# Kernel optimization log

Hardware: AMD Instinct MI355X
Metric: run time of the kernel (lower is better)

Reference implementation:

```python
import jax, jax.numpy as jnp
import numpy as np

D_MODEL = 1024
N_HEADS = 16
HEAD_DIM = D_MODEL // N_HEADS
SEQ_LEN = 2048
D_FF = 4 * D_MODEL
LCC_SCALE = 0.1
LN_EPS = 1e-5
NORM_EPS = 1e-12  # F.normalize eps


def _layer_norm(x, g, b):
    mu = jnp.mean(x, axis=-1, keepdims=True)
    var = jnp.mean(jnp.square(x - mu), axis=-1, keepdims=True)
    return (x - mu) * jax.lax.rsqrt(var + LN_EPS) * g + b


def setup_inputs() -> dict:
    key = jax.random.key(0)
    ks = jax.random.split(key, 8)
    s = 0.02  # weight init scale
    return {
        "x": jax.random.normal(ks[0], (SEQ_LEN, D_MODEL), jnp.float32),
        "lcc_values": jax.random.uniform(ks[1], (SEQ_LEN,), jnp.float32),
        "w_qkv": jax.random.normal(ks[2], (D_MODEL, 3 * D_MODEL), jnp.float32) * s,
        "b_qkv": jnp.zeros((3 * D_MODEL,), jnp.float32),
        "w_out": jax.random.normal(ks[3], (D_MODEL, D_MODEL), jnp.float32) * s,
        "b_out": jnp.zeros((D_MODEL,), jnp.float32),
        "ln1_g": jnp.ones((D_MODEL,), jnp.float32),
        "ln1_b": jnp.zeros((D_MODEL,), jnp.float32),
        "ln2_g": jnp.ones((D_MODEL,), jnp.float32),
        "ln2_b": jnp.zeros((D_MODEL,), jnp.float32),
        "w_ff1": jax.random.normal(ks[4], (D_MODEL, D_FF), jnp.float32) * s,
        "b_ff1": jnp.zeros((D_FF,), jnp.float32),
        "w_ff2": jax.random.normal(ks[5], (D_FF, D_MODEL), jnp.float32) * s,
        "b_ff2": jnp.zeros((D_MODEL,), jnp.float32),
    }


def reference(x, lcc_values, w_qkv, b_qkv, w_out, b_out, ln1_g, ln1_b,
              ln2_g, ln2_b, w_ff1, b_ff1, w_ff2, b_ff2):
    L = x.shape[0]
    scaling = HEAD_DIM ** -0.5

    normed = _layer_norm(x, ln1_g, ln1_b)
    qkv = normed @ w_qkv + b_qkv                      # [L, 3D]
    qkv = qkv.reshape(L, 3, N_HEADS, HEAD_DIM)
    q = jnp.transpose(qkv[:, 0], (1, 0, 2))           # [H, L, d]
    k = jnp.transpose(qkv[:, 1], (1, 0, 2))
    v = jnp.transpose(qkv[:, 2], (1, 0, 2))

    # cosine attention: L2-normalize q, k
    q = q / jnp.maximum(jnp.linalg.norm(q, axis=-1, keepdims=True), NORM_EPS)
    k = k / jnp.maximum(jnp.linalg.norm(k, axis=-1, keepdims=True), NORM_EPS)
    q = q * scaling

    scores = jnp.einsum('hld,hmd->hlm', q, k)         # [H, L, L]
    bias = (lcc_values[:, None] + lcc_values[None, :]) * 0.5 * LCC_SCALE
    scores = jnp.clip(scores + bias[None], -10.0, 10.0)
    probs = jax.nn.softmax(scores, axis=-1)

    attn = jnp.einsum('hlm,hmd->hld', probs, v)       # [H, L, d]
    attn = jnp.transpose(attn, (1, 0, 2)).reshape(L, D_MODEL)
    x = x + (attn @ w_out + b_out)

    normed2 = _layer_norm(x, ln2_g, ln2_b)
    h = jax.nn.gelu(normed2 @ w_ff1 + b_ff1, approximate=False)
    x = x + (h @ w_ff2 + b_ff2)
    return x
```

## Files before the change

### kernel.cpp

```cpp
#include <hip/hip_runtime.h>
#include <hip/hip_bf16.h>

#define D_MODEL 1024
#define SEQ 2048
#define NH 16
#define HD 64
#define DFF 4096

typedef __attribute__((ext_vector_type(8))) __bf16 bf16x8;
typedef __attribute__((ext_vector_type(4))) float f32x4;

__device__ __forceinline__ unsigned short f2bf(float f) {
    union { float f; unsigned u; } v; v.f = f;
    unsigned r = v.u + 0x7fffu + ((v.u >> 16) & 1u);
    return (unsigned short)(r >> 16);
}
__device__ __forceinline__ unsigned pack2(float a, float b) {
    return (unsigned)f2bf(a) | ((unsigned)f2bf(b) << 16);
}
__device__ __forceinline__ float bf2f(unsigned short u) {
    union { unsigned u; float f; } v; v.u = ((unsigned)u) << 16;
    return v.f;
}
__device__ __forceinline__ bf16x8 ld_frag(const unsigned short* p) {
    union { uint4 u; bf16x8 b; } c;
    c.u = *(const uint4*)p;
    return c.b;
}
__device__ __forceinline__ void load16(const float* p, float* v) {
#pragma unroll
    for (int i = 0; i < 4; i++) {
        float4 f = ((const float4*)p)[i];
        v[4*i+0]=f.x; v[4*i+1]=f.y; v[4*i+2]=f.z; v[4*i+3]=f.w;
    }
}

typedef __attribute__((address_space(3))) unsigned lds_u32;
typedef const __attribute__((address_space(1))) unsigned glob_u32;
__device__ __forceinline__ void gl_lds16(const unsigned short* g, unsigned short* l) {
    __builtin_amdgcn_global_load_lds((glob_u32*)g, (lds_u32*)l, 16, 0, 0);
}

#define MFMA16(a,b,c) __builtin_amdgcn_mfma_f32_16x16x32_bf16(a,b,c,0,0,0)

__global__ __launch_bounds__(256) void wcast_t(const float* __restrict__ W,
                                               unsigned short* __restrict__ Wt,
                                               int K, int N) {
    __shared__ unsigned short lt[64][72];
    int t = threadIdx.x;
    int nb = blockIdx.x, kb = blockIdx.y;
    int r = t >> 2, c0 = (t & 3) << 4;
    const float* src = W + (size_t)(kb*64 + r) * N + nb*64 + c0;
    float4 f0 = ((const float4*)src)[0];
    float4 f1 = ((const float4*)src)[1];
    float4 f2 = ((const float4*)src)[2];
    float4 f3 = ((const float4*)src)[3];
    unsigned* dst = (unsigned*)&lt[r][c0];
    dst[0]=pack2(f0.x,f0.y); dst[1]=pack2(f0.z,f0.w);
    dst[2]=pack2(f1.x,f1.y); dst[3]=pack2(f1.z,f1.w);
    dst[4]=pack2(f2.x,f2.y); dst[5]=pack2(f2.z,f2.w);
    dst[6]=pack2(f3.x,f3.y); dst[7]=pack2(f3.z,f3.w);
    __syncthreads();
    int n_ = t >> 2, k0 = (t & 3) << 4;
    unsigned obuf[8];
#pragma unroll
    for (int i = 0; i < 8; i++)
        obuf[i] = (unsigned)lt[k0 + 2*i][n_] | ((unsigned)lt[k0 + 2*i + 1][n_] << 16);
    unsigned short* out = Wt + (size_t)(nb*64 + n_) * K + kb*64 + k0;
    ((uint4*)out)[0] = *(uint4*)&obuf[0];
    ((uint4*)out)[1] = *(uint4*)&obuf[4];
}

__global__ __launch_bounds__(256) void ln_kernel(const float* __restrict__ x,
                                                 const float* __restrict__ g,
                                                 const float* __restrict__ b,
                                                 unsigned short* __restrict__ out) {
    int row = blockIdx.x, t = threadIdx.x;
    float4 v = ((const float4*)(x + (size_t)row * D_MODEL))[t];
    float s  = v.x + v.y + v.z + v.w;
    float sq = v.x*v.x + v.y*v.y + v.z*v.z + v.w*v.w;
#pragma unroll
    for (int m = 1; m < 64; m <<= 1) { s += __shfl_xor(s, m, 64); sq += __shfl_xor(sq, m, 64); }
    __shared__ float ls[4], lq[4];
    int wave = t >> 6, lane = t & 63;
    if (lane == 0) { ls[wave] = s; lq[wave] = sq; }
    __syncthreads();
    s  = ls[0]+ls[1]+ls[2]+ls[3];
    sq = lq[0]+lq[1]+lq[2]+lq[3];
    float mu  = s * (1.0f / D_MODEL);
    float var = sq * (1.0f / D_MODEL) - mu * mu;
    float rs  = rsqrtf(var + 1e-5f);
    int c = t * 4;
    float y0 = (v.x - mu) * rs * g[c+0] + b[c+0];
    float y1 = (v.y - mu) * rs * g[c+1] + b[c+1];
    float y2 = (v.z - mu) * rs * g[c+2] + b[c+2];
    float y3 = (v.w - mu) * rs * g[c+3] + b[c+3];
    unsigned* o = (unsigned*)(out + (size_t)row * D_MODEL + c);
    o[0] = pack2(y0, y1); o[1] = pack2(y2, y3);
}

template<int NP>
__device__ __forceinline__ void reduce_body(const float* __restrict__ res,
                                            const float* __restrict__ bias,
                                            const unsigned short* __restrict__ parts,
                                            float* __restrict__ out,
                                            int MN, int Ndiv4) {
    int i = blockIdx.x * 256 + threadIdx.x;
    float4 r = ((const float4*)res)[i];
    float4 b = ((const float4*)bias)[i & (Ndiv4 - 1)];
    r.x += b.x; r.y += b.y; r.z += b.z; r.w += b.w;
#pragma unroll
    for (int p = 0; p < NP; p++) {
        ushort4 u = ((const ushort4*)(parts + (size_t)p * MN))[i];
        r.x += bf2f(u.x); r.y += bf2f(u.y); r.z += bf2f(u.z); r.w += bf2f(u.w);
    }
    ((float4*)out)[i] = r;
}
__global__ __launch_bounds__(256) void reduce_op(const float* res, const float* bias,
                                                 const unsigned short* parts, float* out,
                                                 int MN, int Ndiv4) {
    reduce_body<2>(res, bias, parts, out, MN, Ndiv4);
}
__global__ __launch_bounds__(256) void reduce_ff2(const float* res, const float* bias,
                                                  const unsigned short* parts, float* out,
                                                  int MN, int Ndiv4) {
    reduce_body<4>(res, bias, parts, out, MN, Ndiv4);
}

template<int TM, int TN, int SPLITK, int GELU, int RES, int OUTBF, int PART>
__device__ __forceinline__ void gemm_body(const unsigned short* __restrict__ A,
                                          const unsigned short* __restrict__ Bt,
                                          const float* __restrict__ bias,
                                          const float* __restrict__ res,
                                          void* __restrict__ C,
                                          int M, int N, int K) {
    constexpr int AI = TM / 32;
    constexpr int BI = TN / 32;
    constexpr int MI = TM / 32;
    constexpr int NI = TN / 32;
    constexpr int HALF = (TM + TN) * 64;
    __shared__ unsigned short smem[2 * HALF];
    int t = threadIdx.x;
    int bn = blockIdx.x, bm = blockIdx.y;
    int kz = (SPLITK > 1) ? blockIdx.z : 0;
    int KS = K / SPLITK;
    int K0 = kz * KS;
    int wave = t >> 6, lane = t & 63;
    int quad = lane >> 4, lr = lane & 15;

    const unsigned short* pa[AI];
    int aoff[AI];
#pragma unroll
    for (int i = 0; i < AI; i++) {
        int rl = wave*(TM/4) + i*8 + (lane >> 3);
        int ss = (lane & 7) ^ (rl & 7);
        pa[i] = A + (size_t)(bm*TM + rl) * K + K0 + ss*8;
        aoff[i] = (wave*(TM/4) + i*8) * 64;
    }
    const unsigned short* pb[BI];
    int boff[BI];
#pragma unroll
    for (int i = 0; i < BI; i++) {
        int rl = wave*(TN/4) + i*8 + (lane >> 3);
        int ss = (lane & 7) ^ (rl & 7);
        pb[i] = Bt + (size_t)(bn*TN + rl) * K + K0 + ss*8;
        boff[i] = TM*64 + (wave*(TN/4) + i*8) * 64;
    }

    int wr = (wave >> 1) * (TM/2), wc = (wave & 1) * (TN/2);
    int foA[2][MI], foB[2][NI];
#pragma unroll
    for (int i = 0; i < MI; i++) {
        int row = wr + i*16 + lr;
        foA[0][i] = row*64 + ((quad     ^ (row & 7)))*8;
        foA[1][i] = row*64 + (((quad+4) ^ (row & 7)))*8;
    }
#pragma unroll
    for (int j = 0; j < NI; j++) {
        int row = wc + j*16 + lr;
        foB[0][j] = TM*64 + row*64 + ((quad     ^ (row & 7)))*8;
        foB[1][j] = TM*64 + row*64 + (((quad+4) ^ (row & 7)))*8;
    }

    f32x4 z = {0.f, 0.f, 0.f, 0.f};
    f32x4 acc[MI][NI];
#pragma unroll
    for (int i = 0; i < MI; i++)
#pragma unroll
        for (int j = 0; j < NI; j++) acc[i][j] = z;

#pragma unroll
    for (int i = 0; i < AI; i++) gl_lds16(pa[i], smem + aoff[i]);
#pragma unroll
    for (int i = 0; i < BI; i++) gl_lds16(pb[i], smem + boff[i]);

    int bo = 0;
    for (int kk = 0; kk < KS; kk += 64) {
        __syncthreads();
        if (kk + 64 < KS) {
            int nb = bo ^ HALF;
#pragma unroll
            for (int i = 0; i < AI; i++) gl_lds16(pa[i] + kk + 64, smem + nb + aoff[i]);
#pragma unroll
            for (int i = 0; i < BI; i++) gl_lds16(pb[i] + kk + 64, smem + nb + boff[i]);
        }
#pragma unroll
        for (int h = 0; h < 2; h++) {
            bf16x8 af[MI], bfr[NI];
#pragma unroll
            for (int i = 0; i < MI; i++) af[i]  = ld_frag(smem + bo + foA[h][i]);
#pragma unroll
            for (int j = 0; j < NI; j++) bfr[j] = ld_frag(smem + bo + foB[h][j]);
#pragma unroll
            for (int i = 0; i < MI; i++)
#pragma unroll
                for (int j = 0; j < NI; j++)
                    acc[i][j] = MFMA16(af[i], bfr[j], acc[i][j]);
        }
        bo ^= HALF;
    }

    if (PART) {
        unsigned short* P = (unsigned short*)C + (size_t)kz * M * N;
#pragma unroll
        for (int i = 0; i < MI; i++)
#pragma unroll
            for (int j = 0; j < NI; j++) {
                int row0 = bm*TM + wr + i*16 + quad*4;
                int col  = bn*TN + wc + j*16 + lr;
#pragma unroll
                for (int r = 0; r < 4; r++)
                    P[(size_t)(row0 + r) * N + col] = f2bf(acc[i][j][r]);
            }
    } else {
#pragma unroll
        for (int i = 0; i < MI; i++)
#pragma unroll
            for (int j = 0; j < NI; j++) {
                int row0 = bm*TM + wr + i*16 + quad*4;
                int col  = bn*TN + wc + j*16 + lr;
                float bv = bias[col];
#pragma unroll
                for (int r = 0; r < 4; r++) {
                    float v = acc[i][j][r] + bv;
                    if (RES)  v += res[(size_t)(row0 + r) * N + col];
                    if (GELU) v = 0.5f * v * (1.0f + erff(v * 0.70710678118654752f));
                    if (OUTBF) ((unsigned short*)C)[(size_t)(row0 + r) * N + col] = f2bf(v);
                    else       ((float*)C)[(size_t)(row0 + r) * N + col] = v;
                }
            }
    }
}

__global__ __launch_bounds__(256) void k_gemm_qkv(const unsigned short* A, const unsigned short* Bt,
                                                  const float* bias, float* C, int M, int N, int K) {
    gemm_body<128,64,1,0,0,0,0>(A, Bt, bias, nullptr, C, M, N, K);
}
__global__ __launch_bounds__(256) void k_gemm_op(const unsigned short* A, const unsigned short* Bt,
                                                 unsigned short* C, int M, int N, int K) {
    gemm_body<128,64,2,0,0,0,1>(A, Bt, nullptr, nullptr, C, M, N, K);
}
__global__ __launch_bounds__(256) void k_gemm_ff1(const unsigned short* A, const unsigned short* Bt,
                                                  const float* bias, unsigned short* C, int M, int N, int K) {
    gemm_body<128,64,1,1,0,1,0>(A, Bt, bias, nullptr, C, M, N, K);
}
__global__ __launch_bounds__(256) void k_gemm_ff2(const unsigned short* A, const unsigned short* Bt,
                                                  unsigned short* C, int M, int N, int K) {
    gemm_body<128,64,4,0,0,0,1>(A, Bt, nullptr, nullptr, C, M, N, K);
}

__global__ __launch_bounds__(256) void qkv_post(const float* __restrict__ qkv,
                                                unsigned short* __restrict__ qn,
                                                unsigned short* __restrict__ kn,
                                                unsigned short* __restrict__ vt) {
    __shared__ unsigned short lv[64][72];
    int h = blockIdx.x, lb = blockIdx.y;
    int t = threadIdx.x;
    int lloc = t >> 2, seg = (t & 3) << 4;
    int lg = lb*64 + lloc;
    const float* row = qkv + (size_t)lg * 3072;
    float vq[16], vk[16], vv[16];
    load16(row + h*64 + seg, vq);
    load16(row + 1024 + h*64 + seg, vk);
    load16(row + 2048 + h*64 + seg, vv);
    float sq = 0.f, sk = 0.f;
#pragma unroll
    for (int i = 0; i < 16; i++) { sq += vq[i]*vq[i]; sk += vk[i]*vk[i]; }
    sq += __shfl_xor(sq, 1, 64); sq += __shfl_xor(sq, 2, 64);
    sk += __shfl_xor(sk, 1, 64); sk += __shfl_xor(sk, 2, 64);
    float scq = 0.125f / fmaxf(sqrtf(sq), 1e-12f);
    float sck = 1.0f   / fmaxf(sqrtf(sk), 1e-12f);
    unsigned* oq = (unsigned*)(qn + ((size_t)h*SEQ + lg)*HD + seg);
    unsigned* ok = (unsigned*)(kn + ((size_t)h*SEQ + lg)*HD + seg);
#pragma unroll
    for (int i = 0; i < 8; i++) {
        oq[i] = pack2(vq[2*i]*scq, vq[2*i+1]*scq);
        ok[i] = pack2(vk[2*i]*sck, vk[2*i+1]*sck);
    }
    unsigned* lvp = (unsigned*)&lv[lloc][seg];
#pragma unroll
    for (int i = 0; i < 8; i++) lvp[i] = pack2(vv[2*i], vv[2*i+1]);
    __syncthreads();
    int dloc = t >> 2, l0 = (t & 3) << 4;
    unsigned obuf[8];
#pragma unroll
    for (int i = 0; i < 8; i++)
        obuf[i] = (unsigned)lv[l0 + 2*i][dloc] | ((unsigned)lv[l0 + 2*i + 1][dloc] << 16);
    unsigned short* ov = vt + ((size_t)h*HD + dloc)*SEQ + lb*64 + l0;
    ((uint4*)ov)[0] = *(uint4*)&obuf[0];
    ((uint4*)ov)[1] = *(uint4*)&obuf[4];
}

#define KSPLIT 2
#define KTILES (SEQ / 64 / KSPLIT)
__global__ __launch_bounds__(256) void attn_kernel(const unsigned short* __restrict__ qn,
                                                   const unsigned short* __restrict__ kn,
                                                   const unsigned short* __restrict__ vt,
                                                   const float* __restrict__ lcc,
                                                   float* __restrict__ num_ws,
                                                   float* __restrict__ den_ws) {
    __shared__ unsigned short lQ[64][72];
    __shared__ unsigned short lK[64][72];
    __shared__ unsigned short lV[64][72];
    __shared__ unsigned short lP[64][72];
    __shared__ float lL[SEQ / KSPLIT];
    int h = blockIdx.x, qb = blockIdx.y, kz = blockIdx.z;
    int t = threadIdx.x;
    int rl = t >> 2, c0 = (t & 3) << 4;
    const unsigned short* pq = qn + ((size_t)h*SEQ + qb*64 + rl)*HD + c0;
    *(uint4*)&lQ[rl][c0]     = ((const uint4*)pq)[0];
    *(uint4*)&lQ[rl][c0 + 8] = ((const uint4*)pq)[1];
    for (int i = t; i < SEQ/KSPLIT; i += 256) lL[i] = 0.05f * lcc[kz*(SEQ/KSPLIT) + i];
    __syncthreads();
    int wave = t >> 6, lane = t & 63, quad = lane >> 4, lr = lane & 15;
    float lqv[4];
#pragma unroll
    for (int r = 0; r < 4; r++) lqv[r] = 0.05f * lcc[qb*64 + wave*16 + quad*4 + r];
    bf16x8 aq0 = ld_frag(&lQ[wave*16 + lr][quad*8]);
    bf16x8 aq1 = ld_frag(&lQ[wave*16 + lr][32 + quad*8]);
    f32x4 z = {0.f, 0.f, 0.f, 0.f};
    f32x4 oacc[4]; oacc[0]=z; oacc[1]=z; oacc[2]=z; oacc[3]=z;
    float den[4] = {0.f, 0.f, 0.f, 0.f};

    const unsigned short* kn0 = kn + (size_t)h*SEQ*HD + (size_t)kz*(SEQ/KSPLIT)*HD;
    const unsigned short* vt0 = vt + (size_t)h*HD*SEQ + kz*(SEQ/KSPLIT);

    for (int kb = 0; kb < KTILES; kb++) {
        __syncthreads();
        const unsigned short* pk = kn0 + (size_t)(kb*64 + rl)*HD + c0;
        uint4 k0v = ((const uint4*)pk)[0], k1v = ((const uint4*)pk)[1];
        const unsigned short* pv = vt0 + (size_t)rl*SEQ + kb*64 + c0;
        uint4 v0v = ((const uint4*)pv)[0], v1v = ((const uint4*)pv)[1];
        *(uint4*)&lK[rl][c0]     = k0v; *(uint4*)&lK[rl][c0 + 8] = k1v;
        *(uint4*)&lV[rl][c0]     = v0v; *(uint4*)&lV[rl][c0 + 8] = v1v;
        __syncthreads();
#pragma unroll
        for (int j = 0; j < 4; j++) {
            bf16x8 b0 = ld_frag(&lK[j*16 + lr][quad*8]);
            bf16x8 b1 = ld_frag(&lK[j*16 + lr][32 + quad*8]);
            f32x4 s = z;
            s = MFMA16(aq0, b0, s);
            s = MFMA16(aq1, b1, s);
            float lm = lL[kb*64 + j*16 + lr];
#pragma unroll
            for (int r = 0; r < 4; r++) {
                float sv = s[r] + lqv[r] + lm;
                sv = fminf(fmaxf(sv, -10.f), 10.f);
                float p = __expf(sv);
                den[r] += p;
                lP[wave*16 + quad*4 + r][j*16 + lr] = f2bf(p);
            }
        }
        bf16x8 ap0 = ld_frag(&lP[wave*16 + lr][quad*8]);
        bf16x8 ap1 = ld_frag(&lP[wave*16 + lr][32 + quad*8]);
#pragma unroll
        for (int j2 = 0; j2 < 4; j2++) {
            bf16x8 b0 = ld_frag(&lV[j2*16 + lr][quad*8]);
            bf16x8 b1 = ld_frag(&lV[j2*16 + lr][32 + quad*8]);
            oacc[j2] = MFMA16(ap0, b0, oacc[j2]);
            oacc[j2] = MFMA16(ap1, b1, oacc[j2]);
        }
    }
#pragma unroll
    for (int r = 0; r < 4; r++)
#pragma unroll
        for (int m = 1; m < 16; m <<= 1) den[r] += __shfl_xor(den[r], m, 64);

    float* nump = num_ws + (((size_t)(h*32 + qb)) * KSPLIT + kz) * 4096;
#pragma unroll
    for (int j2 = 0; j2 < 4; j2++)
#pragma unroll
        for (int r = 0; r < 4; r++)
            nump[(wave*16 + quad*4 + r) * 64 + j2*16 + lr] = oacc[j2][r];
    if (lr == 0) {
        float* denp = den_ws + (((size_t)(h*32 + qb)) * KSPLIT + kz) * 64;
#pragma unroll
        for (int r = 0; r < 4; r++) denp[wave*16 + quad*4 + r] = den[r];
    }
}

__global__ __launch_bounds__(256) void attn_comb(const float* __restrict__ num_ws,
                                                 const float* __restrict__ den_ws,
                                                 unsigned short* __restrict__ attn) {
    int hq = blockIdx.x;
    int h = hq >> 5, qb = hq & 31;
    int t = threadIdx.x;
    int row = t >> 2, col0 = (t & 3) << 4;
    const float* n0 = num_ws + ((size_t)hq * KSPLIT) * 4096 + row*64 + col0;
    const float* n1 = n0 + 4096;
    float d = den_ws[(size_t)hq * KSPLIT * 64 + row] + den_ws[((size_t)hq * KSPLIT + 1) * 64 + row];
    float inv = 1.0f / d;
    unsigned ob[8];
#pragma unroll
    for (int i = 0; i < 4; i++) {
        float4 a = ((const float4*)n0)[i];
        float4 b = ((const float4*)n1)[i];
        ob[2*i]   = pack2((a.x + b.x) * inv, (a.y + b.y) * inv);
        ob[2*i+1] = pack2((a.z + b.z) * inv, (a.w + b.w) * inv);
    }
    unsigned short* op = attn + (size_t)(qb*64 + row) * D_MODEL + h*64 + col0;
    ((uint4*)op)[0] = *(uint4*)&ob[0];
    ((uint4*)op)[1] = *(uint4*)&ob[4];
}

extern "C" void kernel_launch(void* const* d_in, const int* in_sizes, int n_in,
                              void* d_out, int out_size, void* d_ws, size_t ws_size,
                              hipStream_t stream) {
    const float* x      = (const float*)d_in[0];
    const float* lcc    = (const float*)d_in[1];
    const float* w_qkv  = (const float*)d_in[2];
    const float* b_qkv  = (const float*)d_in[3];
    const float* w_out  = (const float*)d_in[4];
    const float* b_out  = (const float*)d_in[5];
    const float* ln1_g  = (const float*)d_in[6];
    const float* ln1_b  = (const float*)d_in[7];
    const float* ln2_g  = (const float*)d_in[8];
    const float* ln2_b  = (const float*)d_in[9];
    const float* w_ff1  = (const float*)d_in[10];
    const float* b_ff1  = (const float*)d_in[11];
    const float* w_ff2  = (const float*)d_in[12];
    const float* b_ff2  = (const float*)d_in[13];

    char* ws = (char*)d_ws;
    unsigned short* wtq  = (unsigned short*)(ws);
    unsigned short* wto  = (unsigned short*)(ws + 6291456);
    unsigned short* wtf1 = (unsigned short*)(ws + 8388608);
    unsigned short* wtf2 = (unsigned short*)(ws + 16777216);
    unsigned short* xn   = (unsigned short*)(ws + 25165824);
    float*          qkvb = (float*)(ws + 29360128);
    float*          x1   = (float*)(ws + 29360128);
    float*          numw = (float*)(ws + 29360128);
    float*          denw = (float*)(ws + 46137344);
    unsigned short* hbuf = (unsigned short*)(ws + 37748736);
    unsigned short* pOP  = (unsigned short*)(ws + 37748736);
    unsigned short* qnb  = (unsigned short*)(ws + 54525952);
    unsigned short* knb  = (unsigned short*)(ws + 58720256);
    unsigned short* vtb  = (unsigned short*)(ws + 62914560);
    unsigned short* pFF2 = (unsigned short*)(ws);
    unsigned short* attnb = xn;
    unsigned short* x2n  = qnb;
    float* outp = (float*)d_out;


    wcast_t<<<dim3(48, 16), 256, 0, stream>>>(w_qkv, wtq, 1024, 3072);
    wcast_t<<<dim3(16, 16), 256, 0, stream>>>(w_out, wto, 1024, 1024);
    wcast_t<<<dim3(64, 16), 256, 0, stream>>>(w_ff1, wtf1, 1024, 4096);
    wcast_t<<<dim3(16, 64), 256, 0, stream>>>(w_ff2, wtf2, 4096, 1024);
    ln_kernel<<<SEQ, 256, 0, stream>>>(x, ln1_g, ln1_b, xn);
    k_gemm_qkv<<<dim3(48, 16), 256, 0, stream>>>(xn, wtq, b_qkv, qkvb, SEQ, 3072, 1024);
    qkv_post<<<dim3(16, 32), 256, 0, stream>>>(qkvb, qnb, knb, vtb);
    attn_kernel<<<dim3(16, 32, KSPLIT), 256, 0, stream>>>(qnb, knb, vtb, lcc, numw, denw);
    attn_comb<<<512, 256, 0, stream>>>(numw, denw, attnb);
    k_gemm_op<<<dim3(16, 16, 2), 256, 0, stream>>>(attnb, wto, pOP, SEQ, 1024, 1024);
    reduce_op<<<SEQ*D_MODEL/1024, 256, 0, stream>>>(x, b_out, pOP, x1, SEQ*D_MODEL, D_MODEL/4);
    ln_kernel<<<SEQ, 256, 0, stream>>>(x1, ln2_g, ln2_b, x2n);
    k_gemm_ff1<<<dim3(64, 16), 256, 0, stream>>>(x2n, wtf1, b_ff1, hbuf, SEQ, 4096, 1024);
    k_gemm_ff2<<<dim3(16, 16, 4), 256, 0, stream>>>(hbuf, wtf2, pFF2, SEQ, 1024, 4096);
    reduce_ff2<<<SEQ*D_MODEL/1024, 256, 0, stream>>>(x1, b_ff2, pFF2, outp, SEQ*D_MODEL, D_MODEL/4);
}
```

Baseline: 283.1 us.

## Fuse QKV post-processing into GEMM epilogue, merge weight casts and reduce+LN

```diff
diff --git a/kernel.cpp b/kernel.cpp
--- a/kernel.cpp
+++ b/kernel.cpp
@@ -27,13 +27,6 @@
     c.u = *(const uint4*)p;
     return c.b;
 }
-__device__ __forceinline__ void load16(const float* p, float* v) {
-#pragma unroll
-    for (int i = 0; i < 4; i++) {
-        float4 f = ((const float4*)p)[i];
-        v[4*i+0]=f.x; v[4*i+1]=f.y; v[4*i+2]=f.z; v[4*i+3]=f.w;
-    }
-}
 
 typedef __attribute__((address_space(3))) unsigned lds_u32;
 typedef const __attribute__((address_space(1))) unsigned glob_u32;
@@ -43,12 +36,18 @@
 
 #define MFMA16(a,b,c) __builtin_amdgcn_mfma_f32_16x16x32_bf16(a,b,c,0,0,0)
 
-__global__ __launch_bounds__(256) void wcast_t(const float* __restrict__ W,
-                                               unsigned short* __restrict__ Wt,
-                                               int K, int N) {
+__global__ __launch_bounds__(256) void wcast_all(const float* __restrict__ wq, const float* __restrict__ wo,
+                                                 const float* __restrict__ wf1, const float* __restrict__ wf2,
+                                                 unsigned short* __restrict__ oq, unsigned short* __restrict__ oo,
+                                                 unsigned short* __restrict__ of1, unsigned short* __restrict__ of2) {
     __shared__ unsigned short lt[64][72];
+    int id = blockIdx.x;
+    const float* W; unsigned short* O; int K, N, nb, kb;
+    if (id < 768)       { W = wq;  O = oq;  K = 1024; N = 3072; nb = id % 48; kb = id / 48; }
+    else if (id < 1024) { id -= 768;  W = wo;  O = oo;  K = 1024; N = 1024; nb = id & 15; kb = id >> 4; }
+    else if (id < 2048) { id -= 1024; W = wf1; O = of1; K = 1024; N = 4096; nb = id & 63; kb = id >> 6; }
+    else                { id -= 2048; W = wf2; O = of2; K = 4096; N = 1024; nb = id & 15; kb = id >> 4; }
     int t = threadIdx.x;
-    int nb = blockIdx.x, kb = blockIdx.y;
     int r = t >> 2, c0 = (t & 3) << 4;
     const float* src = W + (size_t)(kb*64 + r) * N + nb*64 + c0;
     float4 f0 = ((const float4*)src)[0];
@@ -66,7 +65,7 @@
 #pragma unroll
     for (int i = 0; i < 8; i++)
         obuf[i] = (unsigned)lt[k0 + 2*i][n_] | ((unsigned)lt[k0 + 2*i + 1][n_] << 16);
-    unsigned short* out = Wt + (size_t)(nb*64 + n_) * K + kb*64 + k0;
+    unsigned short* out = O + (size_t)(nb*64 + n_) * K + kb*64 + k0;
     ((uint4*)out)[0] = *(uint4*)&obuf[0];
     ((uint4*)out)[1] = *(uint4*)&obuf[4];
 }
@@ -99,75 +98,95 @@
     o[0] = pack2(y0, y1); o[1] = pack2(y2, y3);
 }
 
-template<int NP>
-__device__ __forceinline__ void reduce_body(const float* __restrict__ res,
-                                            const float* __restrict__ bias,
-                                            const unsigned short* __restrict__ parts,
-                                            float* __restrict__ out,
-                                            int MN, int Ndiv4) {
+__global__ __launch_bounds__(256) void reduce_ln(const float* __restrict__ x,
+                                                 const float* __restrict__ bout,
+                                                 const unsigned short* __restrict__ parts,
+                                                 const float* __restrict__ g,
+                                                 const float* __restrict__ b,
+                                                 float* __restrict__ x1,
+                                                 unsigned short* __restrict__ x2n) {
+    int row = blockIdx.x, t = threadIdx.x;
+    int i = row * 256 + t;
+    float4 v = ((const float4*)x)[i];
+    float4 bb = ((const float4*)bout)[t];
+    v.x += bb.x; v.y += bb.y; v.z += bb.z; v.w += bb.w;
+    ushort4 u0 = ((const ushort4*)parts)[i];
+    ushort4 u1 = ((const ushort4*)(parts + (size_t)SEQ*D_MODEL))[i];
+    v.x += bf2f(u0.x) + bf2f(u1.x);
+    v.y += bf2f(u0.y) + bf2f(u1.y);
+    v.z += bf2f(u0.z) + bf2f(u1.z);
+    v.w += bf2f(u0.w) + bf2f(u1.w);
+    ((float4*)x1)[i] = v;
+    float s  = v.x + v.y + v.z + v.w;
+    float sq = v.x*v.x + v.y*v.y + v.z*v.z + v.w*v.w;
+#pragma unroll
+    for (int m = 1; m < 64; m <<= 1) { s += __shfl_xor(s, m, 64); sq += __shfl_xor(sq, m, 64); }
+    __shared__ float ls[4], lq[4];
+    int wave = t >> 6, lane = t & 63;
+    if (lane == 0) { ls[wave] = s; lq[wave] = sq; }
+    __syncthreads();
+    s  = ls[0]+ls[1]+ls[2]+ls[3];
+    sq = lq[0]+lq[1]+lq[2]+lq[3];
+    float mu  = s * (1.0f / D_MODEL);
+    float var = sq * (1.0f / D_MODEL) - mu * mu;
+    float rs  = rsqrtf(var + 1e-5f);
+    int c = t * 4;
+    float y0 = (v.x - mu) * rs * g[c+0] + b[c+0];
+    float y1 = (v.y - mu) * rs * g[c+1] + b[c+1];
+    float y2 = (v.z - mu) * rs * g[c+2] + b[c+2];
+    float y3 = (v.w - mu) * rs * g[c+3] + b[c+3];
+    unsigned* o = (unsigned*)(x2n + (size_t)row * D_MODEL + c);
+    o[0] = pack2(y0, y1); o[1] = pack2(y2, y3);
+}
+
+__global__ __launch_bounds__(256) void reduce_ff2(const float* __restrict__ res,
+                                                  const float* __restrict__ bias,
+                                                  const unsigned short* __restrict__ parts,
+                                                  float* __restrict__ out) {
     int i = blockIdx.x * 256 + threadIdx.x;
     float4 r = ((const float4*)res)[i];
-    float4 b = ((const float4*)bias)[i & (Ndiv4 - 1)];
+    float4 b = ((const float4*)bias)[i & (D_MODEL/4 - 1)];
     r.x += b.x; r.y += b.y; r.z += b.z; r.w += b.w;
 #pragma unroll
-    for (int p = 0; p < NP; p++) {
-        ushort4 u = ((const ushort4*)(parts + (size_t)p * MN))[i];
+    for (int p = 0; p < 4; p++) {
+        ushort4 u = ((const ushort4*)(parts + (size_t)p * SEQ * D_MODEL))[i];
         r.x += bf2f(u.x); r.y += bf2f(u.y); r.z += bf2f(u.z); r.w += bf2f(u.w);
     }
     ((float4*)out)[i] = r;
 }
-__global__ __launch_bounds__(256) void reduce_op(const float* res, const float* bias,
-                                                 const unsigned short* parts, float* out,
-                                                 int MN, int Ndiv4) {
-    reduce_body<2>(res, bias, parts, out, MN, Ndiv4);
-}
-__global__ __launch_bounds__(256) void reduce_ff2(const float* res, const float* bias,
-                                                  const unsigned short* parts, float* out,
-                                                  int MN, int Ndiv4) {
-    reduce_body<4>(res, bias, parts, out, MN, Ndiv4);
-}
-
-template<int TM, int TN, int SPLITK, int GELU, int RES, int OUTBF, int PART>
-__device__ __forceinline__ void gemm_body(const unsigned short* __restrict__ A,
+
+#define TMg 128
+#define TNg 64
+#define SMEM_U16 (2 * (TMg + TNg) * 64)
+__device__ __forceinline__ void gemm_core(const unsigned short* __restrict__ A,
                                           const unsigned short* __restrict__ Bt,
-                                          const float* __restrict__ bias,
-                                          const float* __restrict__ res,
-                                          void* __restrict__ C,
-                                          int M, int N, int K) {
-    constexpr int AI = TM / 32;
-    constexpr int BI = TN / 32;
-    constexpr int MI = TM / 32;
-    constexpr int NI = TN / 32;
-    constexpr int HALF = (TM + TN) * 64;
-    __shared__ unsigned short smem[2 * HALF];
-    int t = threadIdx.x;
-    int bn = blockIdx.x, bm = blockIdx.y;
-    int kz = (SPLITK > 1) ? blockIdx.z : 0;
-    int KS = K / SPLITK;
-    int K0 = kz * KS;
-    int wave = t >> 6, lane = t & 63;
+                                          int K, int K0, int KS, int bm, int bn,
+                                          unsigned short* smem, f32x4 acc[4][2],
+                                          int wave, int lane) {
+    constexpr int AI = 4, BI = 2, MI = 4, NI = 2;
+    constexpr int HALF = (TMg + TNg) * 64;
     int quad = lane >> 4, lr = lane & 15;
 
     const unsigned short* pa[AI];
     int aoff[AI];
 #pragma unroll
     for (int i = 0; i < AI; i++) {
-        int rl = wave*(TM/4) + i*8 + (lane >> 3);
+        int rl = wave*32 + i*8 + (lane >> 3);
         int ss = (lane & 7) ^ (rl & 7);
-        pa[i] = A + (size_t)(bm*TM + rl) * K + K0 + ss*8;
-        aoff[i] = (wave*(TM/4) + i*8) * 64;
+        pa[i] = A + (size_t)(bm*TMg + rl) * K + K0 + ss*8;
+        aoff[i] = (wave*32 + i*8) * 64;
     }
     const unsigned short* pb[BI];
     int boff[BI];
 #pragma unroll
     for (int i = 0; i < BI; i++) {
-        int rl = wave*(TN/4) + i*8 + (lane >> 3);
+        int rl = wave*16 + i*8 + (lane >> 3);
         int ss = (lane & 7) ^ (rl & 7);
-        pb[i] = Bt + (size_t)(bn*TN + rl) * K + K0 + ss*8;
-        boff[i] = TM*64 + (wave*(TN/4) + i*8) * 64;
-    }
-
-    int wr = (wave >> 1) * (TM/2), wc = (wave & 1) * (TN/2);
+        pb[i] = Bt + (size_t)(bn*TNg + rl) * K + K0 + ss*8;
+        boff[i] = TMg*64 + (wave*16 + i*8) * 64;
+    }
+
+    int wr = (wave >> 1) * 64, wc = (wave & 1) * 32;
     int foA[2][MI], foB[2][NI];
 #pragma unroll
     for (int i = 0; i < MI; i++) {
@@ -178,16 +197,9 @@
 #pragma unroll
     for (int j = 0; j < NI; j++) {
         int row = wc + j*16 + lr;
-        foB[0][j] = TM*64 + row*64 + ((quad     ^ (row & 7)))*8;
-        foB[1][j] = TM*64 + row*64 + (((quad+4) ^ (row & 7)))*8;
-    }
-
-    f32x4 z = {0.f, 0.f, 0.f, 0.f};
-    f32x4 acc[MI][NI];
-#pragma unroll
-    for (int i = 0; i < MI; i++)
-#pragma unroll
-        for (int j = 0; j < NI; j++) acc[i][j] = z;
+        foB[0][j] = TMg*64 + row*64 + ((quad     ^ (row & 7)))*8;
+        foB[1][j] = TMg*64 + row*64 + (((quad+4) ^ (row & 7)))*8;
+    }
 
 #pragma unroll
     for (int i = 0; i < AI; i++) gl_lds16(pa[i], smem + aoff[i]);
@@ -219,96 +231,146 @@
         }
         bo ^= HALF;
     }
-
-    if (PART) {
-        unsigned short* P = (unsigned short*)C + (size_t)kz * M * N;
-#pragma unroll
-        for (int i = 0; i < MI; i++)
-#pragma unroll
-            for (int j = 0; j < NI; j++) {
-                int row0 = bm*TM + wr + i*16 + quad*4;
-                int col  = bn*TN + wc + j*16 + lr;
-#pragma unroll
-                for (int r = 0; r < 4; r++)
-                    P[(size_t)(row0 + r) * N + col] = f2bf(acc[i][j][r]);
+}
+
+__device__ __forceinline__ void acc_init(f32x4 acc[4][2]) {
+    f32x4 z = {0.f, 0.f, 0.f, 0.f};
+#pragma unroll
+    for (int i = 0; i < 4; i++) { acc[i][0] = z; acc[i][1] = z; }
+}
+
+__global__ __launch_bounds__(256) void k_gemm_qkv(const unsigned short* __restrict__ A,
+                                                  const unsigned short* __restrict__ Bt,
+                                                  const float* __restrict__ bias,
+                                                  unsigned short* __restrict__ qn,
+                                                  unsigned short* __restrict__ kn,
+                                                  unsigned short* __restrict__ vt) {
+    __shared__ unsigned short smem[SMEM_U16];
+    int t = threadIdx.x;
+    int bn = blockIdx.x, bm = blockIdx.y;
+    int wave = t >> 6, lane = t & 63;
+    int quad = lane >> 4, lr = lane & 15;
+    f32x4 acc[4][2];
+    acc_init(acc);
+    gemm_core(A, Bt, 1024, 0, 1024, bm, bn, smem, acc, wave, lane);
+
+    int wr = (wave >> 1) * 64, wc = (wave & 1) * 32;
+    int sec = bn >> 4, h = bn & 15;
+    float bv0 = bias[bn*64 + wc + lr];
+    float bv1 = bias[bn*64 + wc + 16 + lr];
+#pragma unroll
+    for (int i = 0; i < 4; i++)
+#pragma unroll
+        for (int r = 0; r < 4; r++) { acc[i][0][r] += bv0; acc[i][1][r] += bv1; }
+
+    if (sec < 2) {
+        float* sums = (float*)smem;
+        __syncthreads();
+#pragma unroll
+        for (int i = 0; i < 4; i++)
+#pragma unroll
+            for (int r = 0; r < 4; r++) {
+                float s = acc[i][0][r]*acc[i][0][r] + acc[i][1][r]*acc[i][1][r];
+                s += __shfl_xor(s, 1, 64); s += __shfl_xor(s, 2, 64);
+                s += __shfl_xor(s, 4, 64); s += __shfl_xor(s, 8, 64);
+                if (lr == 0) sums[(wr + i*16 + quad*4 + r)*2 + (wave & 1)] = s;
+            }
+        __syncthreads();
+        unsigned short* dst = (sec == 0) ? qn : kn;
+        float mul = (sec == 0) ? 0.125f : 1.0f;
+#pragma unroll
+        for (int i = 0; i < 4; i++)
+#pragma unroll
+            for (int r = 0; r < 4; r++) {
+                int row = wr + i*16 + quad*4 + r;
+                float tot = sums[row*2] + sums[row*2 + 1];
+                float scale = mul / fmaxf(sqrtf(tot), 1e-12f);
+                size_t base = ((size_t)h*SEQ + bm*128 + row) * HD;
+                dst[base + wc + lr]      = f2bf(acc[i][0][r] * scale);
+                dst[base + wc + 16 + lr] = f2bf(acc[i][1][r] * scale);
             }
     } else {
-#pragma unroll
-        for (int i = 0; i < MI; i++)
-#pragma unroll
-            for (int j = 0; j < NI; j++) {
-                int row0 = bm*TM + wr + i*16 + quad*4;
-                int col  = bn*TN + wc + j*16 + lr;
-                float bv = bias[col];
-#pragma unroll
-                for (int r = 0; r < 4; r++) {
-                    float v = acc[i][j][r] + bv;
-                    if (RES)  v += res[(size_t)(row0 + r) * N + col];
-                    if (GELU) v = 0.5f * v * (1.0f + erff(v * 0.70710678118654752f));
-                    if (OUTBF) ((unsigned short*)C)[(size_t)(row0 + r) * N + col] = f2bf(v);
-                    else       ((float*)C)[(size_t)(row0 + r) * N + col] = v;
-                }
-            }
-    }
-}
-
-__global__ __launch_bounds__(256) void k_gemm_qkv(const unsigned short* A, const unsigned short* Bt,
-                                                  const float* bias, float* C, int M, int N, int K) {
-    gemm_body<128,64,1,0,0,0,0>(A, Bt, bias, nullptr, C, M, N, K);
+        __syncthreads();
+        unsigned short (*lv)[130] = (unsigned short (*)[130])smem;
+#pragma unroll
+        for (int i = 0; i < 4; i++)
+#pragma unroll
+            for (int j = 0; j < 2; j++)
+#pragma unroll
+                for (int r = 0; r < 4; r++)
+                    lv[wc + j*16 + lr][wr + i*16 + quad*4 + r] = f2bf(acc[i][j][r]);
+        __syncthreads();
+        int d = t >> 2, l0 = (t & 3) * 32;
+        unsigned short* ov = vt + ((size_t)(h*HD + d)) * SEQ + bm*128 + l0;
+        ((uint4*)ov)[0] = *(uint4*)&lv[d][l0];
+        ((uint4*)ov)[1] = *(uint4*)&lv[d][l0 + 8];
+        ((uint4*)ov)[2] = *(uint4*)&lv[d][l0 + 16];
+        ((uint4*)ov)[3] = *(uint4*)&lv[d][l0 + 24];
+    }
+}
+
+template<int SPLITK>
+__device__ __forceinline__ void gemm_part(const unsigned short* A, const unsigned short* Bt,
+                                          unsigned short* C, int M, int N, int K) {
+    __shared__ unsigned short smem[SMEM_U16];
+    int t = threadIdx.x;
+    int bn = blockIdx.x, bm = blockIdx.y, kz = blockIdx.z;
+    int wave = t >> 6, lane = t & 63;
+    int quad = lane >> 4, lr = lane & 15;
+    int KS = K / SPLITK;
+    f32x4 acc[4][2];
+    acc_init(acc);
+    gemm_core(A, Bt, K, kz*KS, KS, bm, bn, smem, acc, wave, lane);
+    int wr = (wave >> 1) * 64, wc = (wave & 1) * 32;
+    unsigned short* P = C + (size_t)kz * M * N;
+#pragma unroll
+    for (int i = 0; i < 4; i++)
+#pragma unroll
+        for (int j = 0; j < 2; j++) {
+            int row0 = bm*TMg + wr + i*16 + quad*4;
+            int col  = bn*TNg + wc + j*16 + lr;
+#pragma unroll
+            for (int r = 0; r < 4; r++)
+                P[(size_t)(row0 + r) * N + col] = f2bf(acc[i][j][r]);
+        }
 }
 __global__ __launch_bounds__(256) void k_gemm_op(const unsigned short* A, const unsigned short* Bt,
                                                  unsigned short* C, int M, int N, int K) {
-    gemm_body<128,64,2,0,0,0,1>(A, Bt, nullptr, nullptr, C, M, N, K);
-}
-__global__ __launch_bounds__(256) void k_gemm_ff1(const unsigned short* A, const unsigned short* Bt,
-                                                  const float* bias, unsigned short* C, int M, int N, int K) {
-    gemm_body<128,64,1,1,0,1,0>(A, Bt, bias, nullptr, C, M, N, K);
+    gemm_part<2>(A, Bt, C, M, N, K);
 }
 __global__ __launch_bounds__(256) void k_gemm_ff2(const unsigned short* A, const unsigned short* Bt,
                                                   unsigned short* C, int M, int N, int K) {
-    gemm_body<128,64,4,0,0,0,1>(A, Bt, nullptr, nullptr, C, M, N, K);
-}
-
-__global__ __launch_bounds__(256) void qkv_post(const float* __restrict__ qkv,
-                                                unsigned short* __restrict__ qn,
-                                                unsigned short* __restrict__ kn,
-                                                unsigned short* __restrict__ vt) {
-    __shared__ unsigned short lv[64][72];
-    int h = blockIdx.x, lb = blockIdx.y;
+    gemm_part<4>(A, Bt, C, M, N, K);
+}
+
+__global__ __launch_bounds__(256) void k_gemm_ff1(const unsigned short* __restrict__ A,
+                                                  const unsigned short* __restrict__ Bt,
+                                                  const float* __restrict__ bias,
+                                                  unsigned short* __restrict__ C,
+                                                  int M, int N, int K) {
+    __shared__ unsigned short smem[SMEM_U16];
     int t = threadIdx.x;
-    int lloc = t >> 2, seg = (t & 3) << 4;
-    int lg = lb*64 + lloc;
-    const float* row = qkv + (size_t)lg * 3072;
-    float vq[16], vk[16], vv[16];
-    load16(row + h*64 + seg, vq);
-    load16(row + 1024 + h*64 + seg, vk);
-    load16(row + 2048 + h*64 + seg, vv);
-    float sq = 0.f, sk = 0.f;
-#pragma unroll
-    for (int i = 0; i < 16; i++) { sq += vq[i]*vq[i]; sk += vk[i]*vk[i]; }
-    sq += __shfl_xor(sq, 1, 64); sq += __shfl_xor(sq, 2, 64);
-    sk += __shfl_xor(sk, 1, 64); sk += __shfl_xor(sk, 2, 64);
-    float scq = 0.125f / fmaxf(sqrtf(sq), 1e-12f);
-    float sck = 1.0f   / fmaxf(sqrtf(sk), 1e-12f);
-    unsigned* oq = (unsigned*)(qn + ((size_t)h*SEQ + lg)*HD + seg);
-    unsigned* ok = (unsigned*)(kn + ((size_t)h*SEQ + lg)*HD + seg);
-#pragma unroll
-    for (int i = 0; i < 8; i++) {
-        oq[i] = pack2(vq[2*i]*scq, vq[2*i+1]*scq);
-        ok[i] = pack2(vk[2*i]*sck, vk[2*i+1]*sck);
-    }
-    unsigned* lvp = (unsigned*)&lv[lloc][seg];
-#pragma unroll
-    for (int i = 0; i < 8; i++) lvp[i] = pack2(vv[2*i], vv[2*i+1]);
-    __syncthreads();
-    int dloc = t >> 2, l0 = (t & 3) << 4;
-    unsigned obuf[8];
-#pragma unroll
-    for (int i = 0; i < 8; i++)
-        obuf[i] = (unsigned)lv[l0 + 2*i][dloc] | ((unsigned)lv[l0 + 2*i + 1][dloc] << 16);
-    unsigned short* ov = vt + ((size_t)h*HD + dloc)*SEQ + lb*64 + l0;
-    ((uint4*)ov)[0] = *(uint4*)&obuf[0];
-    ((uint4*)ov)[1] = *(uint4*)&obuf[4];
+    int bn = blockIdx.x, bm = blockIdx.y;
+    int wave = t >> 6, lane = t & 63;
+    int quad = lane >> 4, lr = lane & 15;
+    f32x4 acc[4][2];
+    acc_init(acc);
+    gemm_core(A, Bt, K, 0, K, bm, bn, smem, acc, wave, lane);
+    int wr = (wave >> 1) * 64, wc = (wave & 1) * 32;
+#pragma unroll
+    for (int i = 0; i < 4; i++)
+#pragma unroll
+        for (int j = 0; j < 2; j++) {
+            int row0 = bm*TMg + wr + i*16 + quad*4;
+            int col  = bn*TNg + wc + j*16 + lr;
+            float bv = bias[col];
+#pragma unroll
+            for (int r = 0; r < 4; r++) {
+                float v = acc[i][j][r] + bv;
+                v = 0.5f * v * (1.0f + erff(v * 0.70710678118654752f));
+                C[(size_t)(row0 + r) * N + col] = f2bf(v);
+            }
+        }
 }
 
 #define KSPLIT 2
@@ -447,7 +509,6 @@
     unsigned short* wtf1 = (unsigned short*)(ws + 8388608);
     unsigned short* wtf2 = (unsigned short*)(ws + 16777216);
     unsigned short* xn   = (unsigned short*)(ws + 25165824);
-    float*          qkvb = (float*)(ws + 29360128);
     float*          x1   = (float*)(ws + 29360128);
     float*          numw = (float*)(ws + 29360128);
     float*          denw = (float*)(ws + 46137344);
@@ -462,19 +523,14 @@
     float* outp = (float*)d_out;
 
 
-    wcast_t<<<dim3(48, 16), 256, 0, stream>>>(w_qkv, wtq, 1024, 3072);
-    wcast_t<<<dim3(16, 16), 256, 0, stream>>>(w_out, wto, 1024, 1024);
-    wcast_t<<<dim3(64, 16), 256, 0, stream>>>(w_ff1, wtf1, 1024, 4096);
-    wcast_t<<<dim3(16, 64), 256, 0, stream>>>(w_ff2, wtf2, 4096, 1024);
+    wcast_all<<<3072, 256, 0, stream>>>(w_qkv, w_out, w_ff1, w_ff2, wtq, wto, wtf1, wtf2);
     ln_kernel<<<SEQ, 256, 0, stream>>>(x, ln1_g, ln1_b, xn);
-    k_gemm_qkv<<<dim3(48, 16), 256, 0, stream>>>(xn, wtq, b_qkv, qkvb, SEQ, 3072, 1024);
-    qkv_post<<<dim3(16, 32), 256, 0, stream>>>(qkvb, qnb, knb, vtb);
+    k_gemm_qkv<<<dim3(48, 16), 256, 0, stream>>>(xn, wtq, b_qkv, qnb, knb, vtb);
     attn_kernel<<<dim3(16, 32, KSPLIT), 256, 0, stream>>>(qnb, knb, vtb, lcc, numw, denw);
     attn_comb<<<512, 256, 0, stream>>>(numw, denw, attnb);
     k_gemm_op<<<dim3(16, 16, 2), 256, 0, stream>>>(attnb, wto, pOP, SEQ, 1024, 1024);
-    reduce_op<<<SEQ*D_MODEL/1024, 256, 0, stream>>>(x, b_out, pOP, x1, SEQ*D_MODEL, D_MODEL/4);
-    ln_kernel<<<SEQ, 256, 0, stream>>>(x1, ln2_g, ln2_b, x2n);
+    reduce_ln<<<SEQ, 256, 0, stream>>>(x, b_out, pOP, ln2_g, ln2_b, x1, x2n);
     k_gemm_ff1<<<dim3(64, 16), 256, 0, stream>>>(x2n, wtf1, b_ff1, hbuf, SEQ, 4096, 1024);
     k_gemm_ff2<<<dim3(16, 16, 4), 256, 0, stream>>>(hbuf, wtf2, pFF2, SEQ, 1024, 4096);
-    reduce_ff2<<<SEQ*D_MODEL/1024, 256, 0, stream>>>(x1, b_ff2, pFF2, outp, SEQ*D_MODEL, D_MODEL/4);
-}
+    reduce_ff2<<<SEQ*D_MODEL/1024, 256, 0, stream>>>(x1, b_ff2, pFF2, outp);
+}
```

Measured after the change: 273.4 us. -3.4%, faster.
